# Performance work log

Measured on AMD Instinct MI355X. Metric: run time of the kernel, lower is better.

## Reference

```python
import jax, jax.numpy as jnp
import numpy as np

EMBED = 1024
HEADS = 16
HEAD_DIM = EMBED // HEADS


def setup_inputs() -> dict:
    key = jax.random.key(0)
    ks = jax.random.split(key, 11)
    B, S, D = 2, 2048, EMBED
    scale = 1.0 / np.sqrt(D)
    inp = {
        "q": jax.random.normal(ks[0], (B, S, D), jnp.float32),
        "k": jax.random.normal(ks[1], (B, S, D), jnp.float32),
        "v": jax.random.normal(ks[2], (B, S, D), jnp.float32),
        "Wq": jax.random.normal(ks[3], (D, D), jnp.float32) * scale,
        "bq": jnp.zeros((D,), jnp.float32),
        "Wk": jax.random.normal(ks[4], (D, D), jnp.float32) * scale,
        "bk": jnp.zeros((D,), jnp.float32),
        "Wv": jax.random.normal(ks[5], (D, D), jnp.float32) * scale,
        "bv": jnp.zeros((D,), jnp.float32),
        "Wo": jax.random.normal(ks[6], (D, D), jnp.float32) * scale,
        "bo": jnp.zeros((D,), jnp.float32),
    }
    return inp


def _split_heads(x):
    b, n, c = x.shape
    return x.reshape(b, n, HEADS, c // HEADS).transpose(0, 2, 1, 3)  # [b,h,n,dh]


def reference(q, k, v, Wq, bq, Wk, bk, Wv, bv, Wo, bo):
    qh = _split_heads(q @ Wq + bq)
    kh = _split_heads(k @ Wk + bk)
    vh = _split_heads(v @ Wv + bv)
    scale = 1.0 / jnp.sqrt(jnp.asarray(HEAD_DIM, qh.dtype))
    att = jnp.einsum("bhqd,bhkd->bhqk", qh, kh) * scale
    att = jax.nn.softmax(att, axis=-1)
    out = jnp.einsum("bhqk,bhkd->bhqd", att, vh)
    b, h, n, dh = out.shape
    out = out.transpose(0, 2, 1, 3).reshape(b, n, h * dh)
    return out @ Wo + bo
```

## Files before the change

### kernel.cpp

```cpp
#include <hip/hip_runtime.h>
#include <hip/hip_bf16.h>
#include <stdint.h>

typedef unsigned short u16;
typedef __bf16 bf16x8 __attribute__((ext_vector_type(8)));
typedef float f32x4 __attribute__((ext_vector_type(4)));
typedef float f32x16 __attribute__((ext_vector_type(16)));
typedef unsigned int u32x4 __attribute__((ext_vector_type(4)));
typedef unsigned int u32x2 __attribute__((ext_vector_type(2)));

#define S_LEN 2048
#define DMODEL 1024
#define NHEAD 16
#define DHEAD 64
#define MROWS 4096
#define EXP2SCALE 0.180336880112f

__device__ __forceinline__ u16 f2b(float f) {
  __hip_bfloat16 h = __float2bfloat16(f);
  union { __hip_bfloat16 h; u16 u; } c;
  c.h = h;
  return c.u;
}
__device__ __forceinline__ unsigned int pk2(float lo, float hi) {
  return (unsigned int)f2b(lo) | ((unsigned int)f2b(hi) << 16);
}
__device__ __forceinline__ unsigned int cvtpk(float a, float b) {
  unsigned int r;
  asm("v_cvt_pk_bf16_f32 %0, %1, %2" : "=v"(r) : "v"(a), "v"(b));
  return r;
}
__device__ __forceinline__ void plswap(unsigned int &a, unsigned int &b) {
  auto r = __builtin_amdgcn_permlane32_swap((int)a, (int)b, false, false);
  a = (unsigned int)r[0];
  b = (unsigned int)r[1];
}

__device__ __forceinline__ void gload16(const void* g, void* l) {
  __builtin_amdgcn_global_load_lds(
      (const __attribute__((address_space(1))) unsigned int*)(uintptr_t)g,
      (__attribute__((address_space(3))) unsigned int*)(uintptr_t)l,
      16, 0, 0);
}

__global__ __launch_bounds__(256) void prep(
    const float* __restrict__ q, const float* __restrict__ k, const float* __restrict__ v,
    const float* __restrict__ Wq, const float* __restrict__ Wk,
    const float* __restrict__ Wv, const float* __restrict__ Wo,
    u16* __restrict__ Qx, u16* __restrict__ Kx, u16* __restrict__ Vx,
    u16* __restrict__ Wqt, u16* __restrict__ Wkt,
    u16* __restrict__ Wvt, u16* __restrict__ Wot) {
  __shared__ u16 tile[64][65];
  const int z = blockIdx.z;
  const int tid = threadIdx.x;
  if (z < 3) {
    const float* src = (z == 0) ? q : (z == 1) ? k : v;
    u16* dst = (z == 0) ? Qx : (z == 1) ? Kx : Vx;
    const size_t i8 = ((size_t)blockIdx.x * 256 + tid) * 8;
    float4 a = *(const float4*)(src + i8);
    float4 b = *(const float4*)(src + i8 + 4);
    u16 o[8];
    o[0] = f2b(a.x); o[1] = f2b(a.y); o[2] = f2b(a.z); o[3] = f2b(a.w);
    o[4] = f2b(b.x); o[5] = f2b(b.y); o[6] = f2b(b.z); o[7] = f2b(b.w);
    *(u32x4*)(dst + i8) = *(const u32x4*)o;
    return;
  }
  if (blockIdx.x >= 256) return;
  const int zz = z - 3;
  const float* W = (zz == 0) ? Wq : (zz == 1) ? Wk : (zz == 2) ? Wv : Wo;
  u16* Wt = (zz == 0) ? Wqt : (zz == 1) ? Wkt : (zz == 2) ? Wvt : Wot;
  const int n0 = (blockIdx.x & 15) * 64, k0 = (blockIdx.x >> 4) * 64;
#pragma unroll
  for (int j = 0; j < 16; j++) {
    int idx = j * 256 + tid;
    int r = idx >> 6, c = idx & 63;
    tile[r][c] = f2b(W[(size_t)(k0 + r) * DMODEL + n0 + c]);
  }
  __syncthreads();
#pragma unroll
  for (int j = 0; j < 16; j++) {
    int idx = j * 256 + tid;
    int r = idx >> 6, c = idx & 63;
    Wt[(size_t)(n0 + r) * DMODEL + k0 + c] = tile[c][r];
  }
}

template <int MODE, int BM>
__device__ __forceinline__ void gemm_body(const u16* __restrict__ A,
                                          const u16* __restrict__ Bt,
                                          const float* __restrict__ bias,
                                          void* __restrict__ Cv,
                                          u16* __restrict__ As,
                                          u16* __restrict__ Bs) {
  constexpr int K = DMODEL;
  constexpr int NS = K / 32;
  constexpr int MB = MROWS / BM;
  constexpr int TA = BM / 64;
  constexpr int NI = BM / 32;
  constexpr int ASZ = BM * 32;
  constexpr int BSZ = 128 * 32;
  constexpr int VW = TA + 2;
  const int tid = threadIdx.x;
  const int wave = tid >> 6, lane = tid & 63;
  const int quad = lane >> 4, l15 = lane & 15;
  const int wr = wave >> 1, wc = wave & 1;
  const int lid = blockIdx.y * 8 + blockIdx.x;
  const int sw = (lid & 7) * MB + (lid >> 3);
  const int bcol = sw & 7, brow = sw >> 3;

  f32x4 acc[NI][4] = {};

  auto issue = [&](int b, int s) {
#pragma unroll
    for (int t = 0; t < TA; t++) {
      const int slot = t * 256 + wave * 64 + lane;
      const int row = slot >> 2;
      const int cgc = ((slot & 3) ^ ((row >> 1) & 3)) << 3;
      gload16(A + (size_t)(brow * BM + row) * K + s * 32 + cgc,
              As + b * ASZ + (t * 256 + wave * 64) * 8);
    }
#pragma unroll
    for (int t = 0; t < 2; t++) {
      const int slot = t * 256 + wave * 64 + lane;
      const int row = slot >> 2;
      const int cgc = ((slot & 3) ^ ((row >> 1) & 3)) << 3;
      gload16(Bt + (size_t)(bcol * 128 + row) * K + s * 32 + cgc,
              Bs + b * BSZ + (t * 256 + wave * 64) * 8);
    }
  };

  issue(0, 0);
  issue(1, 1);

#pragma unroll 1
  for (int k = 0; k < NS; ++k) {
    asm volatile("s_waitcnt lgkmcnt(0)" ::: "memory");
    if (k == NS - 1)
      asm volatile("s_waitcnt vmcnt(0)" ::: "memory");
    else
      asm volatile("s_waitcnt vmcnt(%0)" :: "i"(VW) : "memory");
    __builtin_amdgcn_s_barrier();
    __builtin_amdgcn_sched_barrier(0);
    if (k + 2 < NS) issue((k + 2) % 3, k + 2);

    const u16* Ab = As + (k % 3) * ASZ;
    const u16* Bb = Bs + (k % 3) * BSZ;
    bf16x8 af[NI], bfm[4];
#pragma unroll
    for (int i = 0; i < NI; i++)
      af[i] = *(const bf16x8*)(Ab + (wr * (BM / 2) + i * 16 + l15) * 32 +
                               ((quad ^ ((l15 >> 1) & 3)) << 3));
#pragma unroll
    for (int j = 0; j < 4; j++)
      bfm[j] = *(const bf16x8*)(Bb + (wc * 64 + j * 16 + l15) * 32 +
                                ((quad ^ ((l15 >> 1) & 3)) << 3));
    __builtin_amdgcn_s_setprio(1);
#pragma unroll
    for (int i = 0; i < NI; i++)
#pragma unroll
      for (int j = 0; j < 4; j++)
        acc[i][j] = __builtin_amdgcn_mfma_f32_16x16x32_bf16(af[i], bfm[j], acc[i][j], 0, 0, 0);
    __builtin_amdgcn_s_setprio(0);
  }

#pragma unroll
  for (int i = 0; i < NI; i++)
#pragma unroll
    for (int j = 0; j < 4; j++) {
      const int col = bcol * 128 + wc * 64 + j * 16 + l15;
      const float bv = bias[col];
      if (MODE == 2) {
        const int srow = brow * BM + wr * (BM / 2) + i * 16 + quad * 4;
        const int bb = srow >> 11, s = srow & (S_LEN - 1);
        u32x2 pd;
        pd.x = pk2(acc[i][j][0] + bv, acc[i][j][1] + bv);
        pd.y = pk2(acc[i][j][2] + bv, acc[i][j][3] + bv);
        *(u32x2*)((u16*)Cv + ((size_t)(bb * 1024 + col)) * S_LEN + s) = pd;
      } else {
#pragma unroll
        for (int r = 0; r < 4; r++) {
          const int row = brow * BM + wr * (BM / 2) + i * 16 + quad * 4 + r;
          if (MODE == 1)
            ((float*)Cv)[(size_t)row * DMODEL + col] = acc[i][j][r] + bv;
          else if (MODE == 3)
            ((u16*)Cv)[(size_t)row * DMODEL + col] = f2b((acc[i][j][r] + bv) * EXP2SCALE);
          else
            ((u16*)Cv)[(size_t)row * DMODEL + col] = f2b(acc[i][j][r] + bv);
        }
      }
    }
}

__global__ __launch_bounds__(256, 3) void gemm_qkv(
    const u16* __restrict__ Qx, const u16* __restrict__ Kx, const u16* __restrict__ Vx,
    const u16* __restrict__ Wqt, const u16* __restrict__ Wkt, const u16* __restrict__ Wvt,
    const float* __restrict__ bq, const float* __restrict__ bk, const float* __restrict__ bv,
    u16* __restrict__ Qp, u16* __restrict__ Kp, u16* __restrict__ Vt) {
  __shared__ u16 As[3 * 128 * 32];
  __shared__ u16 Bs[3 * 128 * 32];
  const int z = blockIdx.z;
  if (z == 2) {
    gemm_body<2, 128>(Vx, Wvt, bv, Vt, As, Bs);
  } else if (z == 0) {
    gemm_body<3, 128>(Qx, Wqt, bq, Qp, As, Bs);
  } else {
    gemm_body<0, 128>(Kx, Wkt, bk, Kp, As, Bs);
  }
}

__global__ __launch_bounds__(256, 4) void gemm_out(
    const u16* __restrict__ A, const u16* __restrict__ Bt,
    const float* __restrict__ bias, float* __restrict__ C) {
  __shared__ u16 As[3 * 64 * 32];
  __shared__ u16 Bs[3 * 128 * 32];
  gemm_body<1, 64>(A, Bt, bias, C, As, Bs);
}

#define TILE_COMPUTE(ksb, vsb)                                                     \
  do {                                                                             \
    f32x16 sA = {}, sB = {};                                                       \
    __builtin_amdgcn_s_setprio(1);                                                 \
    _Pragma("unroll") for (int c = 0; c < 4; c++) {                                \
      bf16x8 ka0 = *(const bf16x8*)((ksb) + off[c]);                               \
      bf16x8 ka1 = *(const bf16x8*)((ksb) + off[c] + 2048);                        \
      sA = __builtin_amdgcn_mfma_f32_32x32x16_bf16(ka0, qf[c], sA, 0, 0, 0);       \
      sB = __builtin_amdgcn_mfma_f32_32x32x16_bf16(ka1, qf[c], sB, 0, 0, 0);       \
    }                                                                              \
    __builtin_amdgcn_s_setprio(0);                                                 \
    bf16x8 pf[4];                                                                  \
    _Pragma("unroll") for (int kb = 0; kb < 2; kb++) {                             \
      const f32x16 s = kb ? sB : sA;                                               \
      unsigned int cc[8];                                                          \
      _Pragma("unroll") for (int m = 0; m < 8; m++)                                \
        cc[m] = cvtpk(__builtin_amdgcn_exp2f(s[2 * m]),                            \
                      __builtin_amdgcn_exp2f(s[2 * m + 1]));                       \
      plswap(cc[0], cc[2]);                                                        \
      plswap(cc[1], cc[3]);                                                        \
      plswap(cc[4], cc[6]);                                                        \
      plswap(cc[5], cc[7]);                                                        \
      union { unsigned int u[4]; bf16x8 v; } f0, f1;                               \
      f0.u[0] = cc[0]; f0.u[1] = cc[1]; f0.u[2] = cc[2]; f0.u[3] = cc[3];          \
      f1.u[0] = cc[4]; f1.u[1] = cc[5]; f1.u[2] = cc[6]; f1.u[3] = cc[7];          \
      pf[2 * kb] = f0.v; pf[2 * kb + 1] = f1.v;                                    \
    }                                                                              \
    __builtin_amdgcn_s_setprio(1);                                                 \
    _Pragma("unroll") for (int g = 0; g < 4; g++) {                                \
      bf16x8 v0 = *(const bf16x8*)((vsb) + off[g]);                                \
      bf16x8 v1 = *(const bf16x8*)((vsb) + off[g] + 2048);                         \
      lacc  = __builtin_amdgcn_mfma_f32_32x32x16_bf16(pf[g], ones, lacc, 0, 0, 0); \
      oacc0 = __builtin_amdgcn_mfma_f32_32x32x16_bf16(pf[g], v0, oacc0, 0, 0, 0);  \
      oacc1 = __builtin_amdgcn_mfma_f32_32x32x16_bf16(pf[g], v1, oacc1, 0, 0, 0);  \
    }                                                                              \
    __builtin_amdgcn_s_setprio(0);                                                 \
  } while (0)

#define ISSUE(buf, kt)                                                            \
  do {                                                                            \
    if (wave < 4) {                                                               \
      const u16* g = srcK + (size_t)(kt) * 64 * DMODEL;                           \
      _Pragma("unroll") for (int j = 0; j < 4; j++)                               \
        gload16(g + (size_t)j * 8 * DMODEL, dst0 + (buf) * 4096 + j * 512);       \
    } else {                                                                      \
      const u16* g = srcV + (kt) * 64;                                            \
      _Pragma("unroll") for (int j = 0; j < 4; j++)                               \
        gload16(g + (size_t)j * 8 * S_LEN, dst0 + (buf) * 4096 + j * 512);        \
    }                                                                             \
  } while (0)

__global__ __launch_bounds__(512, 4) void attn(const u16* __restrict__ Qp,
                                               const u16* __restrict__ Kp,
                                               const u16* __restrict__ Vt,
                                               u16* __restrict__ Op) {
  __shared__ u16 LB[32768];

  const int tid = threadIdx.x;
  const int wave = tid >> 6, lane = tid & 63;
  const int row31 = lane & 31, hl = lane >> 5;
  const int qg = wave & 3, kh = wave >> 2;

  const int id = blockIdx.x + (blockIdx.y << 4) + (blockIdx.z << 8);
  const int sw = ((id & 7) << 6) + (id >> 3);
  const int qt = sw & 15, h = (sw >> 4) & 15, b = sw >> 8;
  const int s0 = qt * 128;

  const size_t baseK = ((size_t)(b * S_LEN)) * DMODEL + h * DHEAD;
  const size_t baseV = ((size_t)((b * NHEAD + h) * DHEAD)) * S_LEN;

  const int sub = wave & 1, khd = (wave >> 1) & 1;
  const int rl = lane >> 3, cl = lane & 7;
  const int cg8 = (cl ^ rl) << 3;
  const u16* srcK = Kp + baseK + (size_t)(khd * 1024 + sub * 32 + rl) * DMODEL + cg8;
  const u16* srcV = Vt + baseV + (size_t)(sub * 32 + rl) * S_LEN + khd * 1024 + cg8;
  u16* dst0 = LB + (wave >= 4 ? 16384 : 0) + khd * 8192 + (sub * 32) * 64;

  const u16* kcb = LB + kh * 8192;
  const u16* vcb = LB + 16384 + kh * 8192;

  int off[4];
#pragma unroll
  for (int c = 0; c < 4; c++)
    off[c] = row31 * 64 + ((((c << 1) + hl) ^ (row31 & 7)) << 3);

  bf16x8 ones;
  {
    union { u16 a[8]; bf16x8 v; } c;
#pragma unroll
    for (int j = 0; j < 8; j++) c.a[j] = 0x3F80;
    ones = c.v;
  }

  bf16x8 qf[4];
#pragma unroll
  for (int c = 0; c < 4; c++)
    qf[c] = *(const bf16x8*)(Qp +
        ((size_t)(b * S_LEN + s0 + qg * 32 + row31)) * DMODEL +
        h * DHEAD + c * 16 + hl * 8);

  f32x16 oacc0 = {}, oacc1 = {};
  f32x16 lacc = {};

  ISSUE(0, 0);

#pragma unroll 1
  for (int kt = 0; kt < 16; kt += 2) {
    __syncthreads();
    ISSUE(1, kt + 1);
    TILE_COMPUTE(kcb, vcb);
    __syncthreads();
    if (kt + 2 < 16) ISSUE(0, kt + 2);
    TILE_COMPUTE(kcb + 4096, vcb + 4096);
  }

  __syncthreads();
  float* M = ((float*)LB) + qg * 3072;
  if (kh == 1) {
#pragma unroll
    for (int r = 0; r < 16; r++) {
      M[r * 64 + lane]        = oacc0[r];
      M[1024 + r * 64 + lane] = oacc1[r];
      M[2048 + r * 64 + lane] = lacc[r];
    }
  }
  __syncthreads();
  if (kh == 0) {
#pragma unroll
    for (int r = 0; r < 16; r++) {
      const float o0 = oacc0[r] + M[r * 64 + lane];
      const float o1 = oacc1[r] + M[1024 + r * 64 + lane];
      const float ls = lacc[r] + M[2048 + r * 64 + lane];
      const float inv = 1.0f / ls;
      const int qrow = (r & 3) + 8 * (r >> 2) + 4 * hl;
      const size_t rb = ((size_t)(b * S_LEN + s0 + qg * 32 + qrow)) * DMODEL + h * DHEAD;
      Op[rb + row31]      = f2b(o0 * inv);
      Op[rb + 32 + row31] = f2b(o1 * inv);
    }
  }
}

extern "C" void kernel_launch(void* const* d_in, const int* in_sizes, int n_in,
                              void* d_out, int out_size, void* d_ws, size_t ws_size,
                              hipStream_t stream) {
  const float* q  = (const float*)d_in[0];
  const float* k  = (const float*)d_in[1];
  const float* v  = (const float*)d_in[2];
  const float* Wq = (const float*)d_in[3];
  const float* bq = (const float*)d_in[4];
  const float* Wk = (const float*)d_in[5];
  const float* bk = (const float*)d_in[6];
  const float* Wv = (const float*)d_in[7];
  const float* bv = (const float*)d_in[8];
  const float* Wo = (const float*)d_in[9];
  const float* bo = (const float*)d_in[10];

  char* w = (char*)d_ws;
  const size_t WSZ = (size_t)DMODEL * DMODEL * 2;
  const size_t XSZ = (size_t)MROWS * DMODEL * 2;
  u16* Wqt = (u16*)(w);
  u16* Wkt = (u16*)(w + WSZ);
  u16* Wvt = (u16*)(w + 2 * WSZ);
  u16* Wot = (u16*)(w + 3 * WSZ);
  u16* Qx  = (u16*)(w + 4 * WSZ);
  u16* Kx  = (u16*)(w + 4 * WSZ + XSZ);
  u16* Vx  = (u16*)(w + 4 * WSZ + 2 * XSZ);
  u16* Qp  = (u16*)(w + 4 * WSZ + 3 * XSZ);
  u16* Kp  = (u16*)(w + 4 * WSZ + 4 * XSZ);
  u16* Vt  = (u16*)(w + 4 * WSZ + 5 * XSZ);
  u16* Op  = (u16*)(w + 4 * WSZ + 6 * XSZ);

  prep<<<dim3(2048, 1, 7), 256, 0, stream>>>(q, k, v, Wq, Wk, Wv, Wo,
                                             Qx, Kx, Vx, Wqt, Wkt, Wvt, Wot);
  gemm_qkv<<<dim3(8, 32, 3), 256, 0, stream>>>(Qx, Kx, Vx, Wqt, Wkt, Wvt,
                                               bq, bk, bv, Qp, Kp, Vt);
  attn<<<dim3(16, 16, 2), 512, 0, stream>>>(Qp, Kp, Vt, Op);
  gemm_out<<<dim3(8, 64, 1), 256, 0, stream>>>(Op, Wot, bo, (float*)d_out);
}
```

Measured before the change: 211.8 us.

## Switch GEMM to double-buffered LDS pipeline and stage V-transpose stores through LDS

The GEMM main loop drops from a three-stage LDS ring with hand-tuned vmcnt waits to a simple two-stage double buffer guarded by __syncthreads. This shrinks shared memory enough to raise the QKV kernel's launch bounds from 3 to 4 blocks per CU. The V projection epilogue now writes its transposed bf16 tile into LDS with an XOR swizzle and then emits coalesced 16-byte global stores, replacing scattered 8-byte writes. The trade-off is less prefetch depth and a full barrier each k-step, which may expose global load latency.

```diff
diff --git a/kernel.cpp b/kernel.cpp
--- a/kernel.cpp
+++ b/kernel.cpp
@@ -90,8 +90,7 @@
                                           const u16* __restrict__ Bt,
                                           const float* __restrict__ bias,
                                           void* __restrict__ Cv,
-                                          u16* __restrict__ As,
-                                          u16* __restrict__ Bs) {
+                                          u16* __restrict__ LB) {
   constexpr int K = DMODEL;
   constexpr int NS = K / 32;
   constexpr int MB = MROWS / BM;
@@ -99,7 +98,8 @@
   constexpr int NI = BM / 32;
   constexpr int ASZ = BM * 32;
   constexpr int BSZ = 128 * 32;
-  constexpr int VW = TA + 2;
+  u16* As = LB;
+  u16* Bs = LB + 2 * ASZ;
   const int tid = threadIdx.x;
   const int wave = tid >> 6, lane = tid & 63;
   const int quad = lane >> 4, l15 = lane & 15;
@@ -130,21 +130,14 @@
   };
 
   issue(0, 0);
-  issue(1, 1);
 
 #pragma unroll 1
   for (int k = 0; k < NS; ++k) {
-    asm volatile("s_waitcnt lgkmcnt(0)" ::: "memory");
-    if (k == NS - 1)
-      asm volatile("s_waitcnt vmcnt(0)" ::: "memory");
-    else
-      asm volatile("s_waitcnt vmcnt(%0)" :: "i"(VW) : "memory");
-    __builtin_amdgcn_s_barrier();
-    __builtin_amdgcn_sched_barrier(0);
-    if (k + 2 < NS) issue((k + 2) % 3, k + 2);
-
-    const u16* Ab = As + (k % 3) * ASZ;
-    const u16* Bb = Bs + (k % 3) * BSZ;
+    __syncthreads();
+    if (k + 1 < NS) issue((k + 1) & 1, k + 1);
+
+    const u16* Ab = As + (k & 1) * ASZ;
+    const u16* Bb = Bs + (k & 1) * BSZ;
     bf16x8 af[NI], bfm[4];
 #pragma unroll
     for (int i = 0; i < NI; i++)
@@ -163,57 +156,75 @@
     __builtin_amdgcn_s_setprio(0);
   }
 
+  if (MODE == 2) {
+    __syncthreads();
+    u16* Ct = LB;
+#pragma unroll
+    for (int i = 0; i < NI; i++)
+#pragma unroll
+      for (int j = 0; j < 4; j++) {
+        const int n = wc * 64 + j * 16 + l15;
+        const float bv = bias[bcol * 128 + n];
+        const int m = wr * (BM / 2) + i * 16 + quad * 4;
+        const int mc = m >> 3;
+        u32x2 pd;
+        pd.x = pk2(acc[i][j][0] + bv, acc[i][j][1] + bv);
+        pd.y = pk2(acc[i][j][2] + bv, acc[i][j][3] + bv);
+        *(u32x2*)(Ct + n * 128 + ((mc ^ (n & 15)) << 3) + (m & 7)) = pd;
+      }
+    __syncthreads();
+    const int c0 = bcol * 128, sr0 = brow * BM;
+    const int bb = sr0 >> 11, sbase = sr0 & (S_LEN - 1);
+#pragma unroll
+    for (int p = 0; p < 8; p++) {
+      const int idx = p * 256 + tid;
+      const int cl = idx >> 4, sc = idx & 15;
+      *(u32x4*)((u16*)Cv + ((size_t)(bb * 1024 + c0 + cl)) * S_LEN + sbase + sc * 8) =
+          *(const u32x4*)(Ct + cl * 128 + ((sc ^ (cl & 15)) << 3));
+    }
+    return;
+  }
+
 #pragma unroll
   for (int i = 0; i < NI; i++)
 #pragma unroll
     for (int j = 0; j < 4; j++) {
       const int col = bcol * 128 + wc * 64 + j * 16 + l15;
       const float bv = bias[col];
-      if (MODE == 2) {
-        const int srow = brow * BM + wr * (BM / 2) + i * 16 + quad * 4;
-        const int bb = srow >> 11, s = srow & (S_LEN - 1);
-        u32x2 pd;
-        pd.x = pk2(acc[i][j][0] + bv, acc[i][j][1] + bv);
-        pd.y = pk2(acc[i][j][2] + bv, acc[i][j][3] + bv);
-        *(u32x2*)((u16*)Cv + ((size_t)(bb * 1024 + col)) * S_LEN + s) = pd;
-      } else {
-#pragma unroll
-        for (int r = 0; r < 4; r++) {
-          const int row = brow * BM + wr * (BM / 2) + i * 16 + quad * 4 + r;
-          if (MODE == 1)
-            ((float*)Cv)[(size_t)row * DMODEL + col] = acc[i][j][r] + bv;
-          else if (MODE == 3)
-            ((u16*)Cv)[(size_t)row * DMODEL + col] = f2b((acc[i][j][r] + bv) * EXP2SCALE);
-          else
-            ((u16*)Cv)[(size_t)row * DMODEL + col] = f2b(acc[i][j][r] + bv);
-        }
+#pragma unroll
+      for (int r = 0; r < 4; r++) {
+        const int row = brow * BM + wr * (BM / 2) + i * 16 + quad * 4 + r;
+        if (MODE == 1)
+          ((float*)Cv)[(size_t)row * DMODEL + col] = acc[i][j][r] + bv;
+        else if (MODE == 3)
+          ((u16*)Cv)[(size_t)row * DMODEL + col] = f2b((acc[i][j][r] + bv) * EXP2SCALE);
+        else
+          ((u16*)Cv)[(size_t)row * DMODEL + col] = f2b(acc[i][j][r] + bv);
       }
     }
 }
 
-__global__ __launch_bounds__(256, 3) void gemm_qkv(
+__global__ __launch_bounds__(256, 4) void gemm_qkv(
     const u16* __restrict__ Qx, const u16* __restrict__ Kx, const u16* __restrict__ Vx,
     const u16* __restrict__ Wqt, const u16* __restrict__ Wkt, const u16* __restrict__ Wvt,
     const float* __restrict__ bq, const float* __restrict__ bk, const float* __restrict__ bv,
     u16* __restrict__ Qp, u16* __restrict__ Kp, u16* __restrict__ Vt) {
-  __shared__ u16 As[3 * 128 * 32];
-  __shared__ u16 Bs[3 * 128 * 32];
+  __shared__ u16 LB[16384];
   const int z = blockIdx.z;
   if (z == 2) {
-    gemm_body<2, 128>(Vx, Wvt, bv, Vt, As, Bs);
+    gemm_body<2, 128>(Vx, Wvt, bv, Vt, LB);
   } else if (z == 0) {
-    gemm_body<3, 128>(Qx, Wqt, bq, Qp, As, Bs);
+    gemm_body<3, 128>(Qx, Wqt, bq, Qp, LB);
   } else {
-    gemm_body<0, 128>(Kx, Wkt, bk, Kp, As, Bs);
+    gemm_body<0, 128>(Kx, Wkt, bk, Kp, LB);
   }
 }
 
 __global__ __launch_bounds__(256, 4) void gemm_out(
     const u16* __restrict__ A, const u16* __restrict__ Bt,
     const float* __restrict__ bias, float* __restrict__ C) {
-  __shared__ u16 As[3 * 64 * 32];
-  __shared__ u16 Bs[3 * 128 * 32];
-  gemm_body<1, 64>(A, Bt, bias, C, As, Bs);
+  __shared__ u16 LB[12288];
+  gemm_body<1, 64>(A, Bt, bias, C, LB);
 }
 
 #define TILE_COMPUTE(ksb, vsb)                                                     \
```

Result: no change. 209.3 us (-1.2%).
